# Performance work log

Measured on AMD Instinct MI355X. Metric: run time of the kernel, lower is better.

Reference implementation:

```python
import jax, jax.numpy as jnp
import numpy as np

B, N, D, H = 4, 2048, 512, 8
HEAD = D // H
TEMP = 8.0


def setup_inputs() -> dict:
    key = jax.random.key(0)
    k1, k2, k3, k4 = jax.random.split(key, 4)
    return {
        "keys": jax.random.normal(k1, (B, N, D), dtype=jnp.float32),
        "queries": jax.random.normal(k2, (B, N, D), dtype=jnp.float32),
        "values": jax.random.normal(k3, (B, N, D), dtype=jnp.float32),
        "W_comb": jax.random.normal(k4, (D, D), dtype=jnp.float32) * (1.0 / np.sqrt(D)),
        "b_comb": jnp.zeros((D,), dtype=jnp.float32),
    }


def reference(keys, queries, values, W_comb, b_comb):
    b, nk, d = keys.shape
    nq = queries.shape[1]
    h, hd = H, HEAD
    # split heads: (b, n, d) -> (b, n, h, hd)
    k = keys.reshape(b, nk, h, hd)
    q = queries.reshape(b, nq, h, hd)
    v = values.reshape(b, nk, h, hd)
    # scaled dot-product attention per head
    logits = jnp.einsum("bqhd,bkhd->bhqk", q, k) / TEMP  # (b, h, nq, nk)
    w = jax.nn.softmax(logits, axis=-1)
    out = jnp.einsum("bhqk,bkhd->bqhd", w, v).reshape(b, nq, d)
    # head_combine: Linear with bias (torch: x @ W.T + b)
    return out @ W_comb.T + b_comb
```

## Files before the change

### kernel.cpp

```cpp
#include <hip/hip_runtime.h>

#define B_ 4
#define N_ 2048
#define D_ 512
#define H_ 8

typedef __attribute__((ext_vector_type(8))) short bf16x8;
typedef __attribute__((ext_vector_type(4))) short bf16x4;
typedef __attribute__((ext_vector_type(4))) float f32x4;

#define KP 68

__device__ __forceinline__ unsigned short f32_to_bf16(float f) {
  unsigned int u = __float_as_uint(f);
  u += 0x7FFFu + ((u >> 16) & 1u);
  return (unsigned short)(u >> 16);
}

__device__ __forceinline__ unsigned int pack2_bf16(float a, float b) {
#if __has_builtin(__builtin_amdgcn_cvt_pk_bf16_f32)
  typedef __attribute__((ext_vector_type(2))) __bf16 bf16v2;
  bf16v2 r = __builtin_amdgcn_cvt_pk_bf16_f32(a, b);
  return *(unsigned int*)&r;
#else
  return (unsigned int)f32_to_bf16(a) | ((unsigned int)f32_to_bf16(b) << 16);
#endif
}

__device__ __forceinline__ float fast_exp2(float x) {
#if __has_builtin(__builtin_amdgcn_exp2f)
  return __builtin_amdgcn_exp2f(x);
#else
  return exp2f(x);
#endif
}

__device__ __forceinline__ f32x4 mfma16(bf16x4 a, bf16x4 b, f32x4 c) {
#if __has_builtin(__builtin_amdgcn_mfma_f32_16x16x16_bf16)
  return __builtin_amdgcn_mfma_f32_16x16x16_bf16(a, b, c, 0, 0, 0);
#else
  return __builtin_amdgcn_mfma_f32_16x16x16bf16_1k(a, b, c, 0, 0, 0);
#endif
}

__global__ __launch_bounds__(256) void convert_kernel(
    const float* __restrict__ Kf, const float* __restrict__ Qf,
    const float* __restrict__ Vf, const float* __restrict__ Wf,
    unsigned short* __restrict__ Qb, unsigned short* __restrict__ Kb,
    unsigned short* __restrict__ Wb, unsigned short* __restrict__ Vt) {
  __shared__ float tile[64 * 72];
  const int tid = threadIdx.x;
  if (blockIdx.x < 1024) {
    const float qs = 0.125f * 1.4426950408889634f;
    int gid = blockIdx.x * 256 + tid;
    const float4* Q4 = (const float4*)Qf;
    const float4* K4 = (const float4*)Kf;
    for (int i = gid; i < (B_ * N_ * D_) / 4; i += 262144) {
      float4 q = Q4[i];
      ((uint2*)Qb)[i] = make_uint2(pack2_bf16(q.x * qs, q.y * qs),
                                   pack2_bf16(q.z * qs, q.w * qs));
      float4 k = K4[i];
      ((uint2*)Kb)[i] = make_uint2(pack2_bf16(k.x, k.y), pack2_bf16(k.z, k.w));
    }
    if (gid < (D_ * D_) / 4) {
      float4 w = ((const float4*)Wf)[gid];
      ((uint2*)Wb)[gid] = make_uint2(pack2_bf16(w.x, w.y), pack2_bf16(w.z, w.w));
    }
  } else {
    int bid = blockIdx.x - 1024;
    int nt = bid & 31, bh = bid >> 5;
    int b = bh >> 3, h = bh & 7;
    int n0 = nt * 64;
#pragma unroll
    for (int i = 0; i < 4; ++i) {
      int idx = i * 256 + tid;
      int r = idx >> 4, c = idx & 15;
      *(float4*)&tile[r * 72 + c * 4] =
          *(const float4*)(Vf + (size_t)(b * N_ + n0 + r) * D_ + h * 64 + c * 4);
    }
    __syncthreads();
    int d = tid >> 2, c = tid & 3;
    unsigned int o[8];
#pragma unroll
    for (int j = 0; j < 8; ++j)
      o[j] = pack2_bf16(tile[(c * 16 + 2 * j) * 72 + d],
                        tile[(c * 16 + 2 * j + 1) * 72 + d]);
    unsigned short* dst = Vt + ((size_t)bh * 64 + d) * N_ + n0 + c * 16;
    *(bf16x8*)dst = *(bf16x8*)&o[0];
    *(bf16x8*)(dst + 8) = *(bf16x8*)&o[4];
  }
}

__global__ __launch_bounds__(256, 2) void attn_kernel(
    const unsigned short* __restrict__ Qb, const unsigned short* __restrict__ Kb,
    const unsigned short* __restrict__ Vt, unsigned short* __restrict__ Ob) {
  __shared__ unsigned short Kl[2][64 * KP];
  __shared__ unsigned short Vl[2][64 * KP];

  const int tid = threadIdx.x;
  const int w = tid >> 6;
  const int lane = tid & 63;
  const int lr = lane & 15;
  const int lq = lane >> 4;

  const int lid = blockIdx.y * gridDim.x + blockIdx.x;
  const int xcd = lid & 7;
  const int lin = lid >> 3;
  const int bh = xcd * 4 + (lin >> 4);
  const int qb = (lin & 15) * 128;

  const size_t slab = (size_t)(bh >> 3) * N_ * D_ + (size_t)(bh & 7) * 64;
  const unsigned short* kbase = Kb + slab;
  const unsigned short* vtbase = Vt + (size_t)bh * 64 * N_;

  bf16x8 qa[2][2];
#pragma unroll
  for (int g = 0; g < 2; ++g) {
    const unsigned short* qrow =
        Qb + slab + (size_t)(qb + w * 32 + g * 16 + lr) * D_;
    qa[g][0] = *(const bf16x8*)(qrow + 8 * lq);
    qa[g][1] = *(const bf16x8*)(qrow + 32 + 8 * lq);
  }

  f32x4 O[4][2];
#pragma unroll
  for (int i = 0; i < 4; ++i)
#pragma unroll
    for (int g = 0; g < 2; ++g) O[i][g] = (f32x4){0.f, 0.f, 0.f, 0.f};
  float l_g[2] = {0.f, 0.f};

  const int st_r = tid >> 3;
  const int st_c = tid & 7;

  {
    const unsigned short* ksrc = kbase + (size_t)st_r * D_ + st_c * 8;
    bf16x8 a = *(const bf16x8*)ksrc;
    bf16x8 b = *(const bf16x8*)(ksrc + (size_t)32 * D_);
    const unsigned short* vsrc = vtbase + (size_t)st_r * N_ + st_c * 8;
    bf16x8 c = *(const bf16x8*)vsrc;
    bf16x8 d = *(const bf16x8*)(vsrc + (size_t)32 * N_);
    *(bf16x8*)&Kl[0][st_r * KP + st_c * 8] = a;
    *(bf16x8*)&Kl[0][(st_r + 32) * KP + st_c * 8] = b;
    *(bf16x8*)&Vl[0][st_r * KP + st_c * 8] = c;
    *(bf16x8*)&Vl[0][(st_r + 32) * KP + st_c * 8] = d;
  }

  for (int kt = 0; kt < 32; ++kt) {
    const int p = kt & 1;
    __syncthreads();

    bf16x8 nk0, nk1, nv0, nv1;
    const bool more = (kt + 1) < 32;
    if (more) {
      const int kb1 = (kt + 1) * 64;
      const unsigned short* ksrc = kbase + (size_t)(kb1 + st_r) * D_ + st_c * 8;
      nk0 = *(const bf16x8*)ksrc;
      nk1 = *(const bf16x8*)(ksrc + (size_t)32 * D_);
      const unsigned short* vsrc = vtbase + (size_t)st_r * N_ + kb1 + st_c * 8;
      nv0 = *(const bf16x8*)vsrc;
      nv1 = *(const bf16x8*)(vsrc + (size_t)32 * N_);
    }

    f32x4 S[4][2];
    __builtin_amdgcn_s_setprio(1);
#pragma unroll
    for (int nt = 0; nt < 4; ++nt) {
      bf16x8 kf0 = *(const bf16x8*)&Kl[p][(nt * 16 + lr) * KP + 8 * lq];
      bf16x8 kf1 = *(const bf16x8*)&Kl[p][(nt * 16 + lr) * KP + 32 + 8 * lq];
#pragma unroll
      for (int g = 0; g < 2; ++g) {
        S[nt][g] = __builtin_amdgcn_mfma_f32_16x16x32_bf16(
            kf0, qa[g][0], (f32x4){0.f, 0.f, 0.f, 0.f}, 0, 0, 0);
        S[nt][g] = __builtin_amdgcn_mfma_f32_16x16x32_bf16(kf1, qa[g][1],
                                                           S[nt][g], 0, 0, 0);
      }
    }
    __builtin_amdgcn_s_setprio(0);

    bf16x4 pf[4][2];
#pragma unroll
    for (int nt = 0; nt < 4; ++nt)
#pragma unroll
      for (int g = 0; g < 2; ++g) {
        float p0 = fast_exp2(S[nt][g][0]);
        float p1 = fast_exp2(S[nt][g][1]);
        float p2 = fast_exp2(S[nt][g][2]);
        float p3 = fast_exp2(S[nt][g][3]);
        l_g[g] += (p0 + p1) + (p2 + p3);
        uint2 packed = make_uint2(pack2_bf16(p0, p1), pack2_bf16(p2, p3));
        pf[nt][g] = *(bf16x4*)&packed;
      }

    __builtin_amdgcn_s_setprio(1);
#pragma unroll
    for (int dt = 0; dt < 4; ++dt) {
#pragma unroll
      for (int nt = 0; nt < 4; ++nt) {
        bf16x4 vf =
            *(const bf16x4*)&Vl[p][(dt * 16 + lr) * KP + nt * 16 + 4 * lq];
#pragma unroll
        for (int g = 0; g < 2; ++g)
          O[dt][g] = mfma16(vf, pf[nt][g], O[dt][g]);
      }
    }
    __builtin_amdgcn_s_setprio(0);

    if (more) {
      *(bf16x8*)&Kl[1 - p][st_r * KP + st_c * 8] = nk0;
      *(bf16x8*)&Kl[1 - p][(st_r + 32) * KP + st_c * 8] = nk1;
      *(bf16x8*)&Vl[1 - p][st_r * KP + st_c * 8] = nv0;
      *(bf16x8*)&Vl[1 - p][(st_r + 32) * KP + st_c * 8] = nv1;
    }
  }

#pragma unroll
  for (int g = 0; g < 2; ++g) {
    l_g[g] += __shfl_xor(l_g[g], 16);
    l_g[g] += __shfl_xor(l_g[g], 32);
  }

  __syncthreads();
  unsigned short* SR = &Kl[0][0];
#pragma unroll
  for (int g = 0; g < 2; ++g) {
    float linv = 1.0f / l_g[g];
#pragma unroll
    for (int dt = 0; dt < 4; ++dt) {
      float v0 = O[dt][g][0] * linv;
      float v1 = O[dt][g][1] * linv;
      float v2 = O[dt][g][2] * linv;
      float v3 = O[dt][g][3] * linv;
      uint2 packed = make_uint2(pack2_bf16(v0, v1), pack2_bf16(v2, v3));
      *(bf16x4*)&SR[(w * 32 + g * 16 + lr) * KP + dt * 16 + lq * 4] =
          *(bf16x4*)&packed;
    }
  }
  __syncthreads();
  {
    const int row = tid >> 1, half = tid & 1;
    unsigned short* dst = Ob + slab + (size_t)(qb + row) * D_ + half * 32;
    const unsigned short* src = &SR[row * KP + half * 32];
    *(bf16x8*)dst = *(const bf16x8*)src;
    *(bf16x8*)(dst + 8) = *(const bf16x8*)(src + 8);
    *(bf16x8*)(dst + 16) = *(const bf16x8*)(src + 16);
    *(bf16x8*)(dst + 24) = *(const bf16x8*)(src + 24);
  }
}

#define GP 68
__global__ __launch_bounds__(256, 2) void gemm_kernel(
    const unsigned short* __restrict__ A, const unsigned short* __restrict__ Wb,
    const float* __restrict__ bias, float* __restrict__ out) {
  __shared__ unsigned short A_lds[2][64 * GP];
  __shared__ unsigned short W_lds[2][128 * GP];

  const int tid = threadIdx.x;
  const int w = tid >> 6;
  const int lane = tid & 63;
  const int lr = lane & 15;
  const int lq = lane >> 4;

  const int bid = blockIdx.x;
  const int xcd = bid & 7;
  const int lin = bid >> 3;
  const int mb = (xcd * 16 + (lin >> 2)) * 64;
  const int cb = (lin & 3) * 128;

  const int dc = (tid & 7) * 8;
  const int r0 = tid >> 3;

  f32x4 acc[8];
#pragma unroll
  for (int i = 0; i < 8; ++i) acc[i] = (f32x4){0.f, 0.f, 0.f, 0.f};

  {
    *(bf16x8*)&A_lds[0][r0 * GP + dc] =
        *(const bf16x8*)(A + (size_t)(mb + r0) * D_ + dc);
    *(bf16x8*)&A_lds[0][(r0 + 32) * GP + dc] =
        *(const bf16x8*)(A + (size_t)(mb + r0 + 32) * D_ + dc);
#pragma unroll
    for (int j = 0; j < 4; ++j)
      *(bf16x8*)&W_lds[0][(r0 + 32 * j) * GP + dc] =
          *(const bf16x8*)(Wb + (size_t)(cb + r0 + 32 * j) * D_ + dc);
  }

  for (int kt = 0; kt < 8; ++kt) {
    const int p = kt & 1;
    __syncthreads();

    bf16x8 na0, na1, nw0, nw1, nw2, nw3;
    const bool more = (kt + 1) < 8;
    if (more) {
      const int k1 = (kt + 1) * 64;
      na0 = *(const bf16x8*)(A + (size_t)(mb + r0) * D_ + k1 + dc);
      na1 = *(const bf16x8*)(A + (size_t)(mb + r0 + 32) * D_ + k1 + dc);
      nw0 = *(const bf16x8*)(Wb + (size_t)(cb + r0) * D_ + k1 + dc);
      nw1 = *(const bf16x8*)(Wb + (size_t)(cb + r0 + 32) * D_ + k1 + dc);
      nw2 = *(const bf16x8*)(Wb + (size_t)(cb + r0 + 64) * D_ + k1 + dc);
      nw3 = *(const bf16x8*)(Wb + (size_t)(cb + r0 + 96) * D_ + k1 + dc);
    }

    bf16x8 a0 = *(const bf16x8*)&A_lds[p][(w * 16 + lr) * GP + 8 * lq];
    bf16x8 a1 = *(const bf16x8*)&A_lds[p][(w * 16 + lr) * GP + 32 + 8 * lq];
#pragma unroll
    for (int nt = 0; nt < 8; ++nt) {
      bf16x8 b0 = *(const bf16x8*)&W_lds[p][(nt * 16 + lr) * GP + 8 * lq];
      bf16x8 b1 = *(const bf16x8*)&W_lds[p][(nt * 16 + lr) * GP + 32 + 8 * lq];
      acc[nt] = __builtin_amdgcn_mfma_f32_16x16x32_bf16(a0, b0, acc[nt], 0, 0, 0);
      acc[nt] = __builtin_amdgcn_mfma_f32_16x16x32_bf16(a1, b1, acc[nt], 0, 0, 0);
    }

    if (more) {
      *(bf16x8*)&A_lds[1 - p][r0 * GP + dc] = na0;
      *(bf16x8*)&A_lds[1 - p][(r0 + 32) * GP + dc] = na1;
      *(bf16x8*)&W_lds[1 - p][r0 * GP + dc] = nw0;
      *(bf16x8*)&W_lds[1 - p][(r0 + 32) * GP + dc] = nw1;
      *(bf16x8*)&W_lds[1 - p][(r0 + 64) * GP + dc] = nw2;
      *(bf16x8*)&W_lds[1 - p][(r0 + 96) * GP + dc] = nw3;
    }
  }

#pragma unroll
  for (int nt = 0; nt < 8; ++nt) {
    float bc = bias[cb + nt * 16 + lr];
#pragma unroll
    for (int rr = 0; rr < 4; ++rr) {
      int row = mb + w * 16 + lq * 4 + rr;
      out[(size_t)row * D_ + cb + nt * 16 + lr] = acc[nt][rr] + bc;
    }
  }
}

extern "C" void kernel_launch(void* const* d_in, const int* in_sizes, int n_in,
                              void* d_out, int out_size, void* d_ws,
                              size_t ws_size, hipStream_t stream) {
  (void)in_sizes; (void)n_in; (void)out_size; (void)ws_size;
  const float* keys    = (const float*)d_in[0];
  const float* queries = (const float*)d_in[1];
  const float* values  = (const float*)d_in[2];
  const float* W       = (const float*)d_in[3];
  const float* bias    = (const float*)d_in[4];
  float* out = (float*)d_out;

  char* ws = (char*)d_ws;
  unsigned short* Qb = (unsigned short*)(ws);
  unsigned short* Kb = (unsigned short*)(ws + 8388608);
  unsigned short* Vt = (unsigned short*)(ws + 16777216);
  unsigned short* Wb = (unsigned short*)(ws + 25165824);
  unsigned short* Ab = (unsigned short*)(ws + 25690112);

  convert_kernel<<<2048, 256, 0, stream>>>(keys, queries, values, W,
                                           Qb, Kb, Wb, Vt);

  attn_kernel<<<dim3(N_ / 128, B_ * H_), 256, 0, stream>>>(Qb, Kb, Vt, Ab);

  gemm_kernel<<<512, 256, 0, stream>>>(Ab, Wb, bias, out);
}
```

Baseline: 162.2 us.

## Switch attention inner loops to 32x32x16 bf16 MFMA tiles

The attention kernel moves from 16x16 MFMAs to 32x32x16 MFMAs for both the QK^T and PV products. Each wave now owns 32 query columns with 16-float accumulators, and the softmax row sum needs one cross-lane shuffle instead of two. The P operand is rebuilt for the second MFMA by exchanging packed bf16 pairs between the lane halves with shuffles. The LDS row pitch also shrinks from 68 to 66 to change the bank mapping, but 128-bit LDS accesses on odd rows are then no longer 16-byte aligned, which risks split accesses or misaligned-access problems.

```diff
diff --git a/kernel.cpp b/kernel.cpp
--- a/kernel.cpp
+++ b/kernel.cpp
@@ -8,8 +8,10 @@
 typedef __attribute__((ext_vector_type(8))) short bf16x8;
 typedef __attribute__((ext_vector_type(4))) short bf16x4;
 typedef __attribute__((ext_vector_type(4))) float f32x4;
-
-#define KP 68
+typedef __attribute__((ext_vector_type(16))) float f32x16;
+
+#define KP 66
+#define GP 68
 
 __device__ __forceinline__ unsigned short f32_to_bf16(float f) {
   unsigned int u = __float_as_uint(f);
@@ -35,12 +37,8 @@
 #endif
 }
 
-__device__ __forceinline__ f32x4 mfma16(bf16x4 a, bf16x4 b, f32x4 c) {
-#if __has_builtin(__builtin_amdgcn_mfma_f32_16x16x16_bf16)
-  return __builtin_amdgcn_mfma_f32_16x16x16_bf16(a, b, c, 0, 0, 0);
-#else
-  return __builtin_amdgcn_mfma_f32_16x16x16bf16_1k(a, b, c, 0, 0, 0);
-#endif
+__device__ __forceinline__ f32x16 mfma32(bf16x8 a, bf16x8 b, f32x16 c) {
+  return __builtin_amdgcn_mfma_f32_32x32x16_bf16(a, b, c, 0, 0, 0);
 }
 
 __global__ __launch_bounds__(256) void convert_kernel(
@@ -100,8 +98,8 @@
   const int tid = threadIdx.x;
   const int w = tid >> 6;
   const int lane = tid & 63;
-  const int lr = lane & 15;
-  const int lq = lane >> 4;
+  const int qc = lane & 31;
+  const int h = lane >> 5;
 
   const int lid = blockIdx.y * gridDim.x + blockIdx.x;
   const int xcd = lid & 7;
@@ -113,21 +111,20 @@
   const unsigned short* kbase = Kb + slab;
   const unsigned short* vtbase = Vt + (size_t)bh * 64 * N_;
 
-  bf16x8 qa[2][2];
-#pragma unroll
-  for (int g = 0; g < 2; ++g) {
-    const unsigned short* qrow =
-        Qb + slab + (size_t)(qb + w * 32 + g * 16 + lr) * D_;
-    qa[g][0] = *(const bf16x8*)(qrow + 8 * lq);
-    qa[g][1] = *(const bf16x8*)(qrow + 32 + 8 * lq);
-  }
-
-  f32x4 O[4][2];
-#pragma unroll
-  for (int i = 0; i < 4; ++i)
-#pragma unroll
-    for (int g = 0; g < 2; ++g) O[i][g] = (f32x4){0.f, 0.f, 0.f, 0.f};
-  float l_g[2] = {0.f, 0.f};
+  bf16x8 qa[4];
+  {
+    const unsigned short* qrow = Qb + slab + (size_t)(qb + w * 32 + qc) * D_;
+#pragma unroll
+    for (int c = 0; c < 4; ++c)
+      qa[c] = *(const bf16x8*)(qrow + c * 16 + 8 * h);
+  }
+
+  f32x16 O[2];
+#pragma unroll
+  for (int dt = 0; dt < 2; ++dt)
+#pragma unroll
+    for (int i = 0; i < 16; ++i) O[dt][i] = 0.f;
+  float l_g = 0.f;
 
   const int st_r = tid >> 3;
   const int st_c = tid & 7;
@@ -161,46 +158,53 @@
       nv1 = *(const bf16x8*)(vsrc + (size_t)32 * N_);
     }
 
-    f32x4 S[4][2];
+    f32x16 S[2];
     __builtin_amdgcn_s_setprio(1);
 #pragma unroll
-    for (int nt = 0; nt < 4; ++nt) {
-      bf16x8 kf0 = *(const bf16x8*)&Kl[p][(nt * 16 + lr) * KP + 8 * lq];
-      bf16x8 kf1 = *(const bf16x8*)&Kl[p][(nt * 16 + lr) * KP + 32 + 8 * lq];
-#pragma unroll
-      for (int g = 0; g < 2; ++g) {
-        S[nt][g] = __builtin_amdgcn_mfma_f32_16x16x32_bf16(
-            kf0, qa[g][0], (f32x4){0.f, 0.f, 0.f, 0.f}, 0, 0, 0);
-        S[nt][g] = __builtin_amdgcn_mfma_f32_16x16x32_bf16(kf1, qa[g][1],
-                                                           S[nt][g], 0, 0, 0);
+    for (int t = 0; t < 2; ++t) {
+      bf16x8 kf = *(const bf16x8*)&Kl[p][(t * 32 + qc) * KP + 8 * h];
+      S[t] = mfma32(kf, qa[0],
+                    (f32x16){0.f, 0.f, 0.f, 0.f, 0.f, 0.f, 0.f, 0.f,
+                             0.f, 0.f, 0.f, 0.f, 0.f, 0.f, 0.f, 0.f});
+#pragma unroll
+      for (int c = 1; c < 4; ++c) {
+        bf16x8 kfc = *(const bf16x8*)&Kl[p][(t * 32 + qc) * KP + c * 16 + 8 * h];
+        S[t] = mfma32(kfc, qa[c], S[t]);
       }
     }
     __builtin_amdgcn_s_setprio(0);
 
-    bf16x4 pf[4][2];
-#pragma unroll
-    for (int nt = 0; nt < 4; ++nt)
-#pragma unroll
-      for (int g = 0; g < 2; ++g) {
-        float p0 = fast_exp2(S[nt][g][0]);
-        float p1 = fast_exp2(S[nt][g][1]);
-        float p2 = fast_exp2(S[nt][g][2]);
-        float p3 = fast_exp2(S[nt][g][3]);
-        l_g[g] += (p0 + p1) + (p2 + p3);
-        uint2 packed = make_uint2(pack2_bf16(p0, p1), pack2_bf16(p2, p3));
-        pf[nt][g] = *(bf16x4*)&packed;
+    unsigned pw[2][8];
+#pragma unroll
+    for (int t = 0; t < 2; ++t)
+#pragma unroll
+      for (int i = 0; i < 8; ++i) {
+        float e0 = fast_exp2(S[t][2 * i]);
+        float e1 = fast_exp2(S[t][2 * i + 1]);
+        l_g += e0 + e1;
+        pw[t][i] = pack2_bf16(e0, e1);
       }
 
     __builtin_amdgcn_s_setprio(1);
 #pragma unroll
-    for (int dt = 0; dt < 4; ++dt) {
-#pragma unroll
-      for (int nt = 0; nt < 4; ++nt) {
-        bf16x4 vf =
-            *(const bf16x4*)&Vl[p][(dt * 16 + lr) * KP + nt * 16 + 4 * lq];
-#pragma unroll
-        for (int g = 0; g < 2; ++g)
-          O[dt][g] = mfma16(vf, pf[nt][g], O[dt][g]);
+    for (int cg = 0; cg < 4; ++cg) {
+      const int t = cg >> 1;
+      const int o = (cg & 1) * 4;
+      unsigned s0 = h ? pw[t][o + 0] : pw[t][o + 2];
+      unsigned s1 = h ? pw[t][o + 1] : pw[t][o + 3];
+      unsigned r0 = __shfl_xor(s0, 32);
+      unsigned r1 = __shfl_xor(s1, 32);
+      unsigned fr[4];
+      fr[0] = h ? r0 : pw[t][o + 0];
+      fr[1] = h ? r1 : pw[t][o + 1];
+      fr[2] = h ? pw[t][o + 2] : r0;
+      fr[3] = h ? pw[t][o + 3] : r1;
+      bf16x8 pb = *(bf16x8*)fr;
+#pragma unroll
+      for (int dt = 0; dt < 2; ++dt) {
+        bf16x8 vf =
+            *(const bf16x8*)&Vl[p][(dt * 32 + qc) * KP + cg * 16 + 8 * h];
+        O[dt] = mfma32(vf, pb, O[dt]);
       }
     }
     __builtin_amdgcn_s_setprio(0);
@@ -213,27 +217,25 @@
     }
   }
 
-#pragma unroll
-  for (int g = 0; g < 2; ++g) {
-    l_g[g] += __shfl_xor(l_g[g], 16);
-    l_g[g] += __shfl_xor(l_g[g], 32);
-  }
+  l_g += __shfl_xor(l_g, 32);
+  const float linv = 1.0f / l_g;
 
   __syncthreads();
   unsigned short* SR = &Kl[0][0];
-#pragma unroll
-  for (int g = 0; g < 2; ++g) {
-    float linv = 1.0f / l_g[g];
-#pragma unroll
-    for (int dt = 0; dt < 4; ++dt) {
-      float v0 = O[dt][g][0] * linv;
-      float v1 = O[dt][g][1] * linv;
-      float v2 = O[dt][g][2] * linv;
-      float v3 = O[dt][g][3] * linv;
-      uint2 packed = make_uint2(pack2_bf16(v0, v1), pack2_bf16(v2, v3));
-      *(bf16x4*)&SR[(w * 32 + g * 16 + lr) * KP + dt * 16 + lq * 4] =
-          *(bf16x4*)&packed;
-    }
+  {
+    const int row = (w * 32 + qc) * KP;
+#pragma unroll
+    for (int dt = 0; dt < 2; ++dt)
+#pragma unroll
+      for (int qd = 0; qd < 4; ++qd) {
+        const int dbase = dt * 32 + qd * 8 + 4 * h;
+        unsigned a = pack2_bf16(O[dt][4 * qd + 0] * linv,
+                                O[dt][4 * qd + 1] * linv);
+        unsigned b = pack2_bf16(O[dt][4 * qd + 2] * linv,
+                                O[dt][4 * qd + 3] * linv);
+        *(unsigned*)&SR[row + dbase] = a;
+        *(unsigned*)&SR[row + dbase + 2] = b;
+      }
   }
   __syncthreads();
   {
@@ -247,7 +249,6 @@
   }
 }
 
-#define GP 68
 __global__ __launch_bounds__(256, 2) void gemm_kernel(
     const unsigned short* __restrict__ A, const unsigned short* __restrict__ Wb,
     const float* __restrict__ bias, float* __restrict__ out) {
```

Measured after the change: 160.9 us. No clear change (-0.8%).
